# Performance work log

Measured on AMD Instinct MI355X. Metric: run time of the kernel, lower is better.

Reference implementation:

```python
import jax, jax.numpy as jnp
import numpy as np

B, N = 4, 1024
DIM, DEPTH, HEADS, DHEAD, MLP = 512, 6, 8, 64, 2048
INNER = HEADS * DHEAD
SCALE = DHEAD ** -0.5
EPS = 1e-5


def setup_inputs() -> dict:
    key = jax.random.key(0)
    ks = jax.random.split(key, 16)
    w = lambda k, shape: (jax.random.normal(k, shape, jnp.float32) * 0.02)
    D = DEPTH
    return {
        "g": jax.random.normal(ks[0], (B, N, DIM), jnp.float32),
        "x": jax.random.normal(ks[1], (B, N, DIM), jnp.float32),
        # PreNorm + SelfAttention
        "ln1_s": jnp.ones((D, DIM)), "ln1_b": jnp.zeros((D, DIM)),
        "Wqkv": w(ks[2], (D, DIM, 3 * INNER)),
        "Wo_sa": w(ks[3], (D, INNER, DIM)), "bo_sa": jnp.zeros((D, DIM)),
        # RelationalCrossAttention
        "lng_s": jnp.ones((D, DIM)), "lng_b": jnp.zeros((D, DIM)),
        "lnx_s": jnp.ones((D, DIM)), "lnx_b": jnp.zeros((D, DIM)),
        "Wq": w(ks[4], (D, DIM, INNER)),
        "Wk": w(ks[5], (D, DIM, INNER)),
        "Wv": w(ks[6], (D, DIM, INNER)), "bv": jnp.zeros((D, INNER)),
        "Wo_ca": w(ks[7], (D, INNER, DIM)), "bo_ca": jnp.zeros((D, DIM)),
        # PreNorm + FeedForward (same module applied twice per layer)
        "lnf_s": jnp.ones((D, DIM)), "lnf_b": jnp.zeros((D, DIM)),
        "W1": w(ks[8], (D, DIM, MLP)), "b1": jnp.zeros((D, MLP)),
        "W2": w(ks[9], (D, MLP, DIM)), "b2": jnp.zeros((D, DIM)),
    }


def _ln(t, s, b):
    m = t.mean(-1, keepdims=True)
    v = ((t - m) ** 2).mean(-1, keepdims=True)
    return (t - m) / jnp.sqrt(v + EPS) * s + b


def _split_heads(t):  # [b, n, h*d] -> [b, h, n, d]
    b, n, _ = t.shape
    return t.reshape(b, n, HEADS, DHEAD).transpose(0, 2, 1, 3)


def _merge_heads(t):  # [b, h, n, d] -> [b, n, h*d]
    b, h, n, d = t.shape
    return t.transpose(0, 2, 1, 3).reshape(b, n, h * d)


def _attend(q, k, v):
    dots = jnp.einsum('bhnd,bhmd->bhnm', q, k) * SCALE
    attn = jax.nn.softmax(jnp.nan_to_num(dots, nan=-jnp.inf), axis=-1)
    attn = jnp.nan_to_num(attn)  # nan_to_num(0.0) post-softmax as in source
    return jnp.einsum('bhnm,bhmd->bhnd', attn, jnp.nan_to_num(v))


def reference(g, x, ln1_s, ln1_b, Wqkv, Wo_sa, bo_sa, lng_s, lng_b, lnx_s, lnx_b,
              Wq, Wk, Wv, bv, Wo_ca, bo_ca, lnf_s, lnf_b, W1, b1, W2, b2):
    for i in range(DEPTH):
        def ff(t):
            h = jax.nn.gelu(_ln(t, lnf_s[i], lnf_b[i]) @ W1[i] + b1[i], approximate=False)
            return h @ W2[i] + b2[i]
        # relational cross attention: q,k from g, v from x
        gn = _ln(g, lng_s[i], lng_b[i])
        xn = _ln(x, lnx_s[i], lnx_b[i])
        q = _split_heads(gn @ Wq[i])
        k = _split_heads(gn @ Wk[i])
        v = _split_heads(xn @ Wv[i] + bv[i])
        x = _merge_heads(_attend(q, k, v)) @ Wo_ca[i] + bo_ca[i] + x
        x = ff(x) + x
        # pre-norm self attention (skip connection enabled)
        sn = _ln(x, ln1_s[i], ln1_b[i])
        qkv = sn @ Wqkv[i]
        qs, ks_, vs = jnp.split(qkv, 3, axis=-1)
        sa = _merge_heads(_attend(_split_heads(qs), _split_heads(ks_), _split_heads(vs)))
        x = sa @ Wo_sa[i] + bo_sa[i] + x
        x = ff(x) + x
    return x
```

## Files before the change

### kernel.cpp

```cpp
#include <hip/hip_runtime.h>
#include <hip/hip_bf16.h>
#include <cstdint>
#include <cstddef>

#define DEV __device__ __forceinline__

using f32x4 = __attribute__((ext_vector_type(4))) float;
using bfx8  = __attribute__((ext_vector_type(8))) __bf16;
using s16x8 = __attribute__((ext_vector_type(8))) short;

DEV uint16_t f2bf(float f) {
    union { float f; uint32_t u; } x; x.f = f;
    uint32_t r = x.u + 0x7fffu + ((x.u >> 16) & 1u);
    return (uint16_t)(r >> 16);
}

DEV float gelu_exact(float v) {
    return 0.5f * v * (1.0f + erff(v * 0.70710678118654752f));
}

DEV f32x4 mfma16(s16x8 a, s16x8 b, f32x4 c) {
    return __builtin_amdgcn_mfma_f32_16x16x32_bf16(
        __builtin_bit_cast(bfx8, a), __builtin_bit_cast(bfx8, b), c, 0, 0, 0);
}

DEV void async_lds16(const void* g, void* l) {
    __builtin_amdgcn_global_load_lds(
        (const __attribute__((address_space(1))) uint32_t*)g,
        (__attribute__((address_space(3))) uint32_t*)l, 16, 0, 0);
}

template<int N> DEV void wait_vmcnt() {
    if constexpr (N == 0)      asm volatile("s_waitcnt vmcnt(0)" ::: "memory");
    else if constexpr (N == 4) asm volatile("s_waitcnt vmcnt(4)" ::: "memory");
    else static_assert(N == 0 || N == 4, "add vmcnt literal");
}
#define SBAR      asm volatile("s_barrier" ::: "memory")
#define LGKM0     asm volatile("s_waitcnt lgkmcnt(0)" ::: "memory")
#define SCHED0    __builtin_amdgcn_sched_barrier(0)

template<int HAS_SB>
__global__ __launch_bounds__(256)
void ln_t(const float* __restrict__ in, const float* __restrict__ sc,
          const float* __restrict__ bi, uint16_t* __restrict__ out)
{
    const int lane = threadIdx.x & 63;
    const size_t row = (size_t)blockIdx.x * 4 + (threadIdx.x >> 6);
    const float* p = in + row * 512 + lane * 8;
    float4 a = *(const float4*)p;
    float4 b4 = *(const float4*)(p + 4);
    float v[8] = {a.x, a.y, a.z, a.w, b4.x, b4.y, b4.z, b4.w};
    float s = 0.f, sq = 0.f;
#pragma unroll
    for (int j = 0; j < 8; ++j) { s += v[j]; sq += v[j] * v[j]; }
#pragma unroll
    for (int o = 1; o < 64; o <<= 1) { s += __shfl_xor(s, o); sq += __shfl_xor(sq, o); }
    const float mean = s * (1.0f / 512.0f);
    const float var  = sq * (1.0f / 512.0f) - mean * mean;
    const float rstd = rsqrtf(var + 1e-5f);
    const int c = lane * 8;
    uint16_t o8[8];
#pragma unroll
    for (int j = 0; j < 8; ++j) {
        float z = (v[j] - mean) * rstd;
        if (HAS_SB) z = z * sc[c + j] + bi[c + j];
        o8[j] = f2bf(z);
    }
    uint4 pk;
    pk.x = (uint32_t)o8[0] | ((uint32_t)o8[1] << 16);
    pk.y = (uint32_t)o8[2] | ((uint32_t)o8[3] << 16);
    pk.z = (uint32_t)o8[4] | ((uint32_t)o8[5] << 16);
    pk.w = (uint32_t)o8[6] | ((uint32_t)o8[7] << 16);
    *reinterpret_cast<uint4*>(out + row * 512 + c) = pk;
}

__global__ __launch_bounds__(256)
void wtrans(const float* __restrict__ W, uint16_t* __restrict__ WT, int K, int N,
            size_t lstride, int row0, const float* __restrict__ kscale)
{
    __shared__ float tile[32][33];
    const int l = blockIdx.z;
    const int k0 = blockIdx.x * 32, n0 = blockIdx.y * 32;
    const float* Wl = W + (size_t)l * K * N;
    uint16_t* WTl = WT + (size_t)l * lstride;
    const int tx = threadIdx.x, ty = threadIdx.y;
#pragma unroll
    for (int j = 0; j < 4; ++j) {
        const int k = k0 + ty + j * 8;
        float w = Wl[(size_t)k * N + n0 + tx];
        if (kscale) w *= kscale[l * K + k];
        tile[ty + j * 8][tx] = w;
    }
    __syncthreads();
#pragma unroll
    for (int j = 0; j < 4; ++j)
        WTl[(size_t)(row0 + n0 + ty + j * 8) * K + k0 + tx] = f2bf(tile[tx][ty + j * 8]);
}

__global__ __launch_bounds__(256)
void bfold(const float* __restrict__ b, const float* __restrict__ Wq,
           const float* __restrict__ Wk, float* __restrict__ out)
{
    const int n = blockIdx.x * 256 + threadIdx.x;
    const int l = blockIdx.y, sel = blockIdx.z;
    const float* bb = b + l * 512;
    const float* W = (sel ? Wk : Wq) + (size_t)l * 512 * 512;
    float s = 0.f;
    for (int k = 0; k < 512; ++k) s += bb[k] * W[(size_t)k * 512 + n];
    out[l * 1024 + sel * 512 + n] = s;
}

template<int BM, int BN, int NWR, int NWC, int MINW,
         int HAS_BIAS, int HAS_RESID, int DO_GELU, int OUT_BF16, int OUT_VT>
__global__ __launch_bounds__(NWR * NWC * 64, MINW)
void gemm7(const uint16_t* __restrict__ A, const uint16_t* __restrict__ BT,
           const float* __restrict__ bias, const float* __restrict__ resid,
           void* __restrict__ outp, uint16_t* __restrict__ vt,
           int M, int N, int K)
{
    constexpr int NT = NWR * NWC * 64;
    constexpr int WM = BM / NWR, WN = BN / NWC;
    constexpr int FM = WM / 16, FN = WN / 16;
    constexpr int ASLOTS = 8 * BM, BSLOTS = 8 * BN, TOT = ASLOTS + BSLOTS;
    constexpr int S = TOT / NT;
    static_assert(S == 4, "vmcnt literal assumes S==4");
    __shared__ uint16_t As[2][ASLOTS * 8];
    __shared__ uint16_t Bs[2][BSLOTS * 8];
    const int tid = threadIdx.x, lane = tid & 63;
    const int w = tid >> 6, wr = w / NWC, wc = w % NWC;
    const int kg = lane >> 4, lr = lane & 15;
    const int nbn = N / BN, nbm = M / BM;
    const int rect_m = nbm >> 1, rect_n = nbn >> 2;
    const int xcd = blockIdx.x & 7, c = blockIdx.x >> 3;
    const int bm = (xcd >> 2) * rect_m + c / rect_n;
    const int bn = (xcd & 3) * rect_n + c % rect_n;
    const size_t m0 = (size_t)bm * BM;
    const size_t n0 = (size_t)bn * BN;

    auto stage = [&](int b, int k0) {
#pragma unroll
        for (int j = 0; j < S; ++j) {
            const int s = j * NT + tid;
            if (s < ASLOTS) {
                const int sub = s / BM, row = s % BM;
                async_lds16(A + (m0 + row) * K + k0 + sub * 8, &As[b][s * 8]);
            } else {
                const int s2 = s - ASLOTS;
                const int sub = s2 / BN, row = s2 % BN;
                async_lds16(BT + (n0 + row) * K + k0 + sub * 8, &Bs[b][s2 * 8]);
            }
        }
    };

    f32x4 acc[FM][FN] = {};
    const int nt = K / 64;
    stage(0, 0);
    stage(1, 64);
    int cur = 0;
    for (int t = 0; t < nt; ++t) {
        if (t < nt - 1) wait_vmcnt<S>(); else wait_vmcnt<0>();
        SBAR;
        s16x8 af[2][FM], bf[2][FN];
#pragma unroll
        for (int ks = 0; ks < 2; ++ks) {
#pragma unroll
            for (int i = 0; i < FM; ++i)
                af[ks][i] = *(const s16x8*)&As[cur][((ks * 4 + kg) * BM + wr * WM + i * 16 + lr) * 8];
#pragma unroll
            for (int j = 0; j < FN; ++j)
                bf[ks][j] = *(const s16x8*)&Bs[cur][((ks * 4 + kg) * BN + wc * WN + j * 16 + lr) * 8];
        }
        __builtin_amdgcn_s_setprio(1);
#pragma unroll
        for (int ks = 0; ks < 2; ++ks)
#pragma unroll
            for (int i = 0; i < FM; ++i)
#pragma unroll
                for (int j = 0; j < FN; ++j)
                    acc[i][j] = mfma16(af[ks][i], bf[ks][j], acc[i][j]);
        __builtin_amdgcn_s_setprio(0);
        LGKM0; SCHED0;
        SBAR;
        if (t + 2 < nt) stage(cur, (t + 2) * 64);
        cur ^= 1;
    }
    if (OUT_VT == 1 || (OUT_VT == 2 && n0 >= 1024)) {
#pragma unroll
        for (int i = 0; i < FM; ++i) {
            const size_t rbase = m0 + wr * WM + i * 16 + kg * 4;
            const int b = (int)(rbase >> 10), nloc = (int)(rbase & 1023);
#pragma unroll
            for (int j = 0; j < FN; ++j) {
                const int col = (int)n0 + wc * WN + j * 16 + lr;
                const int c2 = (OUT_VT == 2) ? col - 1024 : col;
                const float bval = HAS_BIAS ? bias[c2] : 0.0f;
                const int h = c2 >> 6, d = c2 & 63;
                ushort4 pk;
                pk.x = f2bf(acc[i][j][0] + bval);
                pk.y = f2bf(acc[i][j][1] + bval);
                pk.z = f2bf(acc[i][j][2] + bval);
                pk.w = f2bf(acc[i][j][3] + bval);
                *(ushort4*)&vt[((size_t)(b * 8 + h) * 64 + d) * 1024 + nloc] = pk;
            }
        }
        return;
    }
#pragma unroll
    for (int i = 0; i < FM; ++i) {
        const size_t rbase = m0 + wr * WM + i * 16 + kg * 4;
#pragma unroll
        for (int j = 0; j < FN; ++j) {
            const size_t col = n0 + wc * WN + j * 16 + lr;
            const float bval = HAS_BIAS ? bias[col] : 0.0f;
#pragma unroll
            for (int r = 0; r < 4; ++r) {
                const size_t row = rbase + r;
                float v = acc[i][j][r] + bval;
                if (DO_GELU)  v = gelu_exact(v);
                if (HAS_RESID) v += resid[row * (size_t)N + col];
                if (OUT_BF16) ((uint16_t*)outp)[row * (size_t)N + col] = f2bf(v);
                else          ((float*)outp)[row * (size_t)N + col] = v;
            }
        }
    }
}

__global__ __launch_bounds__(256)
void attn_flash(const uint16_t* __restrict__ Qb, const uint16_t* __restrict__ Kb,
                const uint16_t* __restrict__ Vt, uint16_t* __restrict__ Ob,
                int qstride, int kstride, int qoff, int koff)
{
    __shared__ uint16_t Ks[2][4096];
    __shared__ uint16_t Vs[2][4096];
    __shared__ uint16_t Pb[4][1024];
    const int tid = threadIdx.x, lane = tid & 63, w = tid >> 6;
    const int kg = lane >> 4, lr = lane & 15;
    const int bh = blockIdx.y, b = bh >> 3, h = bh & 7;
    const int q0 = blockIdx.x * 64;
    const float CEXP = 0.125f * 1.44269504f;

    s16x8 aq0, aq1;
    {
        const size_t qrow = (size_t)b * 1024 + q0 + w * 16 + lr;
        const uint16_t* qp = Qb + qrow * qstride + qoff + h * 64 + kg * 8;
        aq0 = *(const s16x8*)qp;
        aq1 = *(const s16x8*)(qp + 32);
    }
    const uint16_t* kbase = Kb + (size_t)b * 1024 * kstride + koff + h * 64;
    const uint16_t* vbase = Vt + (size_t)bh * 65536;

    float l_r[4] = {0.f, 0.f, 0.f, 0.f};
    f32x4 acc[4] = {};

    auto stage = [&](int buf, int kv0) {
#pragma unroll
        for (int j = 0; j < 2; ++j) {
            const int s = j * 256 + tid;
            const int sub = s >> 6, row = s & 63;
            async_lds16(kbase + (size_t)(kv0 + row) * kstride + sub * 8, &Ks[buf][s * 8]);
            async_lds16(vbase + (size_t)row * 1024 + kv0 + sub * 8,      &Vs[buf][s * 8]);
        }
    };

    stage(0, 0);
    __syncthreads();
    int cur = 0;
    for (int t = 0; t < 16; ++t) {
        if (t < 15) stage(cur ^ 1, (t + 1) * 64);
        f32x4 s4[4];
        __builtin_amdgcn_s_setprio(1);
#pragma unroll
        for (int ni = 0; ni < 4; ++ni) {
            s16x8 bk0 = *(const s16x8*)&Ks[cur][(kg * 64 + ni * 16 + lr) * 8];
            s16x8 bk1 = *(const s16x8*)&Ks[cur][((4 + kg) * 64 + ni * 16 + lr) * 8];
            f32x4 z = {};
            z = mfma16(aq0, bk0, z);
            z = mfma16(aq1, bk1, z);
            s4[ni] = z;
        }
        __builtin_amdgcn_s_setprio(0);
#pragma unroll
        for (int ni = 0; ni < 4; ++ni) {
            const int slotb = (ni * 2 + (lr >> 3)) * 16 + kg * 4;
#pragma unroll
            for (int r = 0; r < 4; ++r) {
                const float pe = __builtin_amdgcn_exp2f(s4[ni][r] * CEXP);
                l_r[r] += pe;
                Pb[w][(slotb + r) * 8 + (lr & 7)] = f2bf(pe);
            }
        }
        s16x8 ap0 = *(const s16x8*)&Pb[w][(kg * 16 + lr) * 8];
        s16x8 ap1 = *(const s16x8*)&Pb[w][((4 + kg) * 16 + lr) * 8];
        __builtin_amdgcn_s_setprio(1);
#pragma unroll
        for (int ni = 0; ni < 4; ++ni) {
            s16x8 bv0 = *(const s16x8*)&Vs[cur][(kg * 64 + ni * 16 + lr) * 8];
            s16x8 bv1 = *(const s16x8*)&Vs[cur][((4 + kg) * 64 + ni * 16 + lr) * 8];
            acc[ni] = mfma16(ap0, bv0, acc[ni]);
            acc[ni] = mfma16(ap1, bv1, acc[ni]);
        }
        __builtin_amdgcn_s_setprio(0);
        __syncthreads();
        cur ^= 1;
    }
    float linv[4];
#pragma unroll
    for (int r = 0; r < 4; ++r) {
        float l = l_r[r];
        l += __shfl_xor(l, 1); l += __shfl_xor(l, 2);
        l += __shfl_xor(l, 4); l += __shfl_xor(l, 8);
        linv[r] = 1.0f / l;
    }
#pragma unroll
    for (int ni = 0; ni < 4; ++ni)
#pragma unroll
        for (int r = 0; r < 4; ++r) {
            const float v = acc[ni][r] * linv[r];
            const size_t row = (size_t)b * 1024 + q0 + w * 16 + kg * 4 + r;
            Ob[row * 512 + h * 64 + ni * 16 + lr] = f2bf(v);
        }
}

extern "C" void kernel_launch(void* const* d_in, const int* in_sizes, int n_in,
                              void* d_out, int out_size, void* d_ws, size_t ws_size,
                              hipStream_t stream)
{
    (void)in_sizes; (void)n_in; (void)out_size; (void)ws_size;
    const float* g     = (const float*)d_in[0];
    const float* x0    = (const float*)d_in[1];
    const float* ln1_s = (const float*)d_in[2];
    const float* ln1_b = (const float*)d_in[3];
    const float* Wqkv  = (const float*)d_in[4];
    const float* Wo_sa = (const float*)d_in[5];
    const float* bo_sa = (const float*)d_in[6];
    const float* lng_s = (const float*)d_in[7];
    const float* lng_b = (const float*)d_in[8];
    const float* lnx_s = (const float*)d_in[9];
    const float* lnx_b = (const float*)d_in[10];
    const float* Wq    = (const float*)d_in[11];
    const float* Wk    = (const float*)d_in[12];
    const float* Wv    = (const float*)d_in[13];
    const float* bv    = (const float*)d_in[14];
    const float* Wo_ca = (const float*)d_in[15];
    const float* bo_ca = (const float*)d_in[16];
    const float* lnf_s = (const float*)d_in[17];
    const float* lnf_b = (const float*)d_in[18];
    const float* W1    = (const float*)d_in[19];
    const float* b1    = (const float*)d_in[20];
    const float* W2    = (const float*)d_in[21];
    const float* b2    = (const float*)d_in[22];

    float* x = (float*)d_out;

    char* p = (char*)d_ws;
    auto carve = [&](size_t n) { char* r = p; p += (n + 255) & ~(size_t)255; return r; };
    uint16_t* WqkT  = (uint16_t*)carve(6ull * 1024 * 512 * 2);
    uint16_t* WvT   = (uint16_t*)carve(6ull * 512 * 512 * 2);
    uint16_t* WocaT = (uint16_t*)carve(6ull * 512 * 512 * 2);
    uint16_t* WqkvT = (uint16_t*)carve(6ull * 1536 * 512 * 2);
    uint16_t* WosaT = (uint16_t*)carve(6ull * 512 * 512 * 2);
    uint16_t* W1T   = (uint16_t*)carve(6ull * 2048 * 512 * 2);
    uint16_t* W2T   = (uint16_t*)carve(6ull * 512 * 2048 * 2);
    float*    bqk   = (float*)carve(6144ull * 4);
    uint16_t* zg    = (uint16_t*)carve(4096ull * 512 * 2);
    uint16_t* qkall = (uint16_t*)carve(4096ull * 6144 * 2);
    uint16_t* xn    = (uint16_t*)carve(4096ull * 512 * 2);
    uint16_t* qkvu  = (uint16_t*)carve(4096ull * 1536 * 2);
    uint16_t* vt    = (uint16_t*)carve(32ull * 64 * 1024 * 2);
    uint16_t* ab    = (uint16_t*)carve(4096ull * 512 * 2);
    uint16_t* hb    = (uint16_t*)carve(4096ull * 2048 * 2);

    dim3 tb(32, 8);
    wtrans<<<dim3(16, 16, 6), tb, 0, stream>>>(Wq,    WqkT,  512, 512,  1024ull * 512, 0,   lng_s);
    wtrans<<<dim3(16, 16, 6), tb, 0, stream>>>(Wk,    WqkT,  512, 512,  1024ull * 512, 512, lng_s);
    wtrans<<<dim3(16, 16, 6), tb, 0, stream>>>(Wv,    WvT,   512, 512,  512ull * 512, 0, nullptr);
    wtrans<<<dim3(16, 16, 6), tb, 0, stream>>>(Wo_ca, WocaT, 512, 512,  512ull * 512, 0, nullptr);
    wtrans<<<dim3(16, 48, 6), tb, 0, stream>>>(Wqkv,  WqkvT, 512, 1536, 1536ull * 512, 0, nullptr);
    wtrans<<<dim3(16, 16, 6), tb, 0, stream>>>(Wo_sa, WosaT, 512, 512,  512ull * 512, 0, nullptr);
    wtrans<<<dim3(16, 64, 6), tb, 0, stream>>>(W1,    W1T,   512, 2048, 2048ull * 512, 0, nullptr);
    wtrans<<<dim3(64, 16, 6), tb, 0, stream>>>(W2,    W2T,   2048, 512, 2048ull * 512, 0, nullptr);
    bfold<<<dim3(2, 6, 2), 256, 0, stream>>>(lng_b, Wq, Wk, bqk);

    hipMemcpyAsync(x, x0, 4096ull * 512 * 4, hipMemcpyDeviceToDevice, stream);

    ln_t<0><<<1024, 256, 0, stream>>>(g, nullptr, nullptr, zg);
    ln_t<1><<<1024, 256, 0, stream>>>(x, lnx_s, lnx_b, xn);
    gemm7<128, 128, 2, 4, 4, 1, 0, 0, 1, 0><<<1536, 512, 0, stream>>>(
        zg, WqkT, bqk, nullptr, qkall, nullptr, 4096, 6144, 512);

    const dim3 ga(16, 32);

    for (int l = 0; l < 6; ++l) {
        const size_t o512 = (size_t)l * 512, oW = (size_t)l * 512 * 512;
        const size_t oW1 = (size_t)l * 2048 * 512, oWqkv = (size_t)l * 1536 * 512;
        const size_t o2048 = (size_t)l * 2048;

        gemm7<64, 64, 2, 2, 4, 1, 0, 0, 0, 1><<<512, 256, 0, stream>>>(
            xn, WvT + oW, bv + o512, nullptr, nullptr, vt, 4096, 512, 512);
        attn_flash<<<ga, 256, 0, stream>>>(qkall, qkall, vt, ab, 6144, 6144,
                                           l * 1024, l * 1024 + 512);
        gemm7<64, 64, 2, 2, 4, 1, 1, 0, 0, 0><<<512, 256, 0, stream>>>(
            ab, WocaT + oW, bo_ca + o512, x, x, nullptr, 4096, 512, 512);

        ln_t<1><<<1024, 256, 0, stream>>>(x, lnf_s + o512, lnf_b + o512, xn);
        gemm7<128, 128, 2, 4, 4, 1, 0, 1, 1, 0><<<512, 512, 0, stream>>>(
            xn, W1T + oW1, b1 + o2048, nullptr, hb, nullptr, 4096, 2048, 512);
        gemm7<64, 64, 2, 2, 4, 1, 1, 0, 0, 0><<<512, 256, 0, stream>>>(
            hb, W2T + oW1, b2 + o512, x, x, nullptr, 4096, 512, 2048);
        ln_t<1><<<1024, 256, 0, stream>>>(x, ln1_s + o512, ln1_b + o512, xn);

        gemm7<128, 128, 2, 4, 4, 0, 0, 0, 1, 2><<<384, 512, 0, stream>>>(
            xn, WqkvT + oWqkv, nullptr, nullptr, qkvu, vt, 4096, 1536, 512);
        attn_flash<<<ga, 256, 0, stream>>>(qkvu, qkvu, vt, ab, 1536, 1536, 0, 512);
        gemm7<64, 64, 2, 2, 4, 1, 1, 0, 0, 0><<<512, 256, 0, stream>>>(
            ab, WosaT + oW, bo_sa + o512, x, x, nullptr, 4096, 512, 512);

        ln_t<1><<<1024, 256, 0, stream>>>(x, lnf_s + o512, lnf_b + o512, xn);
        gemm7<128, 128, 2, 4, 4, 1, 0, 1, 1, 0><<<512, 512, 0, stream>>>(
            xn, W1T + oW1, b1 + o2048, nullptr, hb, nullptr, 4096, 2048, 512);
        gemm7<64, 64, 2, 2, 4, 1, 1, 0, 0, 0><<<512, 256, 0, stream>>>(
            hb, W2T + oW1, b2 + o512, x, x, nullptr, 4096, 512, 2048);
        if (l < 5)
            ln_t<1><<<1024, 256, 0, stream>>>(x, lnx_s + o512 + 512, lnx_b + o512 + 512, xn);
    }
}
```

Baseline: 1.591 ms.

## Replace double-buffered async GEMM with single-buffered BK=32 occupancy-oriented GEMM

Replaces the 2-stage double-buffered GEMM with a single-buffered loop over K in steps of 32. The old kernel used explicit vmcnt waits, raw barriers and priority hints; the new loop uses a plain __syncthreads before and after each compute step. All tiles now run with 4 waves in a 2x2 layout, and the launch-bounds minimum-waves hint rises to 3 or 5 for more occupancy. The aim is to cut LDS use and raise occupancy so other blocks can hide memory latency. In exchange, each block no longer overlaps its own loads with compute and pays twice as many barriers per unit of K.

New measurement: 1.666 ms. 4.7% more time.

```diff
diff --git a/kernel.cpp b/kernel.cpp
--- a/kernel.cpp
+++ b/kernel.cpp
@@ -29,15 +29,6 @@
         (const __attribute__((address_space(1))) uint32_t*)g,
         (__attribute__((address_space(3))) uint32_t*)l, 16, 0, 0);
 }
-
-template<int N> DEV void wait_vmcnt() {
-    if constexpr (N == 0)      asm volatile("s_waitcnt vmcnt(0)" ::: "memory");
-    else if constexpr (N == 4) asm volatile("s_waitcnt vmcnt(4)" ::: "memory");
-    else static_assert(N == 0 || N == 4, "add vmcnt literal");
-}
-#define SBAR      asm volatile("s_barrier" ::: "memory")
-#define LGKM0     asm volatile("s_waitcnt lgkmcnt(0)" ::: "memory")
-#define SCHED0    __builtin_amdgcn_sched_barrier(0)
 
 template<int HAS_SB>
 __global__ __launch_bounds__(256)
@@ -110,24 +101,22 @@
     out[l * 1024 + sel * 512 + n] = s;
 }
 
-template<int BM, int BN, int NWR, int NWC, int MINW,
+template<int BM, int BN, int MINW,
          int HAS_BIAS, int HAS_RESID, int DO_GELU, int OUT_BF16, int OUT_VT>
-__global__ __launch_bounds__(NWR * NWC * 64, MINW)
-void gemm7(const uint16_t* __restrict__ A, const uint16_t* __restrict__ BT,
+__global__ __launch_bounds__(256, MINW)
+void gemm9(const uint16_t* __restrict__ A, const uint16_t* __restrict__ BT,
            const float* __restrict__ bias, const float* __restrict__ resid,
            void* __restrict__ outp, uint16_t* __restrict__ vt,
            int M, int N, int K)
 {
-    constexpr int NT = NWR * NWC * 64;
-    constexpr int WM = BM / NWR, WN = BN / NWC;
+    constexpr int WM = BM / 2, WN = BN / 2;
     constexpr int FM = WM / 16, FN = WN / 16;
-    constexpr int ASLOTS = 8 * BM, BSLOTS = 8 * BN, TOT = ASLOTS + BSLOTS;
-    constexpr int S = TOT / NT;
-    static_assert(S == 4, "vmcnt literal assumes S==4");
-    __shared__ uint16_t As[2][ASLOTS * 8];
-    __shared__ uint16_t Bs[2][BSLOTS * 8];
+    constexpr int ASLOTS = 4 * BM, BSLOTS = 4 * BN, TOT = ASLOTS + BSLOTS;
+    constexpr int S = TOT / 256;
+    __shared__ uint16_t As[ASLOTS * 8];
+    __shared__ uint16_t Bs[BSLOTS * 8];
     const int tid = threadIdx.x, lane = tid & 63;
-    const int w = tid >> 6, wr = w / NWC, wc = w % NWC;
+    const int w = tid >> 6, wr = w >> 1, wc = w & 1;
     const int kg = lane >> 4, lr = lane & 15;
     const int nbn = N / BN, nbm = M / BM;
     const int rect_m = nbm >> 1, rect_n = nbn >> 2;
@@ -137,52 +126,34 @@
     const size_t m0 = (size_t)bm * BM;
     const size_t n0 = (size_t)bn * BN;
 
-    auto stage = [&](int b, int k0) {
+    f32x4 acc[FM][FN] = {};
+    for (int k0 = 0; k0 < K; k0 += 32) {
 #pragma unroll
         for (int j = 0; j < S; ++j) {
-            const int s = j * NT + tid;
+            const int s = j * 256 + tid;
             if (s < ASLOTS) {
                 const int sub = s / BM, row = s % BM;
-                async_lds16(A + (m0 + row) * K + k0 + sub * 8, &As[b][s * 8]);
+                async_lds16(A + (m0 + row) * K + k0 + sub * 8, &As[s * 8]);
             } else {
                 const int s2 = s - ASLOTS;
                 const int sub = s2 / BN, row = s2 % BN;
-                async_lds16(BT + (n0 + row) * K + k0 + sub * 8, &Bs[b][s2 * 8]);
+                async_lds16(BT + (n0 + row) * K + k0 + sub * 8, &Bs[s2 * 8]);
             }
         }
-    };
-
-    f32x4 acc[FM][FN] = {};
-    const int nt = K / 64;
-    stage(0, 0);
-    stage(1, 64);
-    int cur = 0;
-    for (int t = 0; t < nt; ++t) {
-        if (t < nt - 1) wait_vmcnt<S>(); else wait_vmcnt<0>();
-        SBAR;
-        s16x8 af[2][FM], bf[2][FN];
-#pragma unroll
-        for (int ks = 0; ks < 2; ++ks) {
-#pragma unroll
-            for (int i = 0; i < FM; ++i)
-                af[ks][i] = *(const s16x8*)&As[cur][((ks * 4 + kg) * BM + wr * WM + i * 16 + lr) * 8];
+        __syncthreads();
+        s16x8 af[FM], bf[FN];
+#pragma unroll
+        for (int i = 0; i < FM; ++i)
+            af[i] = *(const s16x8*)&As[(kg * BM + wr * WM + i * 16 + lr) * 8];
+#pragma unroll
+        for (int j = 0; j < FN; ++j)
+            bf[j] = *(const s16x8*)&Bs[(kg * BN + wc * WN + j * 16 + lr) * 8];
+#pragma unroll
+        for (int i = 0; i < FM; ++i)
 #pragma unroll
             for (int j = 0; j < FN; ++j)
-                bf[ks][j] = *(const s16x8*)&Bs[cur][((ks * 4 + kg) * BN + wc * WN + j * 16 + lr) * 8];
-        }
-        __builtin_amdgcn_s_setprio(1);
-#pragma unroll
-        for (int ks = 0; ks < 2; ++ks)
-#pragma unroll
-            for (int i = 0; i < FM; ++i)
-#pragma unroll
-                for (int j = 0; j < FN; ++j)
-                    acc[i][j] = mfma16(af[ks][i], bf[ks][j], acc[i][j]);
-        __builtin_amdgcn_s_setprio(0);
-        LGKM0; SCHED0;
-        SBAR;
-        if (t + 2 < nt) stage(cur, (t + 2) * 64);
-        cur ^= 1;
+                acc[i][j] = mfma16(af[i], bf[j], acc[i][j]);
+        __syncthreads();
     }
     if (OUT_VT == 1 || (OUT_VT == 2 && n0 >= 1024)) {
 #pragma unroll
@@ -385,7 +356,7 @@
 
     ln_t<0><<<1024, 256, 0, stream>>>(g, nullptr, nullptr, zg);
     ln_t<1><<<1024, 256, 0, stream>>>(x, lnx_s, lnx_b, xn);
-    gemm7<128, 128, 2, 4, 4, 1, 0, 0, 1, 0><<<1536, 512, 0, stream>>>(
+    gemm9<128, 128, 3, 1, 0, 0, 1, 0><<<1536, 256, 0, stream>>>(
         zg, WqkT, bqk, nullptr, qkall, nullptr, 4096, 6144, 512);
 
     const dim3 ga(16, 32);
@@ -395,30 +366,30 @@
         const size_t oW1 = (size_t)l * 2048 * 512, oWqkv = (size_t)l * 1536 * 512;
         const size_t o2048 = (size_t)l * 2048;
 
-        gemm7<64, 64, 2, 2, 4, 1, 0, 0, 0, 1><<<512, 256, 0, stream>>>(
+        gemm9<64, 64, 5, 1, 0, 0, 0, 1><<<512, 256, 0, stream>>>(
             xn, WvT + oW, bv + o512, nullptr, nullptr, vt, 4096, 512, 512);
         attn_flash<<<ga, 256, 0, stream>>>(qkall, qkall, vt, ab, 6144, 6144,
                                            l * 1024, l * 1024 + 512);
-        gemm7<64, 64, 2, 2, 4, 1, 1, 0, 0, 0><<<512, 256, 0, stream>>>(
+        gemm9<64, 64, 5, 1, 1, 0, 0, 0><<<512, 256, 0, stream>>>(
             ab, WocaT + oW, bo_ca + o512, x, x, nullptr, 4096, 512, 512);
 
         ln_t<1><<<1024, 256, 0, stream>>>(x, lnf_s + o512, lnf_b + o512, xn);
-        gemm7<128, 128, 2, 4, 4, 1, 0, 1, 1, 0><<<512, 512, 0, stream>>>(
+        gemm9<128, 128, 3, 1, 0, 1, 1, 0><<<512, 256, 0, stream>>>(
             xn, W1T + oW1, b1 + o2048, nullptr, hb, nullptr, 4096, 2048, 512);
-        gemm7<64, 64, 2, 2, 4, 1, 1, 0, 0, 0><<<512, 256, 0, stream>>>(
+        gemm9<64, 64, 5, 1, 1, 0, 0, 0><<<512, 256, 0, stream>>>(
             hb, W2T + oW1, b2 + o512, x, x, nullptr, 4096, 512, 2048);
         ln_t<1><<<1024, 256, 0, stream>>>(x, ln1_s + o512, ln1_b + o512, xn);
 
-        gemm7<128, 128, 2, 4, 4, 0, 0, 0, 1, 2><<<384, 512, 0, stream>>>(
+        gemm9<128, 128, 3, 0, 0, 0, 1, 2><<<384, 256, 0, stream>>>(
             xn, WqkvT + oWqkv, nullptr, nullptr, qkvu, vt, 4096, 1536, 512);
         attn_flash<<<ga, 256, 0, stream>>>(qkvu, qkvu, vt, ab, 1536, 1536, 0, 512);
-        gemm7<64, 64, 2, 2, 4, 1, 1, 0, 0, 0><<<512, 256, 0, stream>>>(
+        gemm9<64, 64, 5, 1, 1, 0, 0, 0><<<512, 256, 0, stream>>>(
             ab, WosaT + oW, bo_sa + o512, x, x, nullptr, 4096, 512, 512);
 
         ln_t<1><<<1024, 256, 0, stream>>>(x, lnf_s + o512, lnf_b + o512, xn);
-        gemm7<128, 128, 2, 4, 4, 1, 0, 1, 1, 0><<<512, 512, 0, stream>>>(
+        gemm9<128, 128, 3, 1, 0, 1, 1, 0><<<512, 256, 0, stream>>>(
             xn, W1T + oW1, b1 + o2048, nullptr, hb, nullptr, 4096, 2048, 512);
-        gemm7<64, 64, 2, 2, 4, 1, 1, 0, 0, 0><<<512, 256, 0, stream>>>(
+        gemm9<64, 64, 5, 1, 1, 0, 0, 0><<<512, 256, 0, stream>>>(
             hb, W2T + oW1, b2 + o512, x, x, nullptr, 4096, 512, 2048);
         if (l < 5)
             ln_t<1><<<1024, 256, 0, stream>>>(x, lnx_s + o512 + 512, lnx_b + o512 + 512, xn);
```
